# Optimization experiments

Hardware: AMD Instinct MI355X
Metric: run time of the kernel (lower is better)

Reference implementation:

```python
import jax, jax.numpy as jnp
import numpy as np

B, L, D = 32768, 256, 16  # batch, chain length, bond dim; physical dim d=2


def setup_inputs() -> dict:
    key = jax.random.key(0)
    k_phi, k_first, k_mid, k_last = jax.random.split(key, 4)
    scale = 1.0 / np.sqrt(2.0 * D)  # variance-preserving chain
    phi_batch = jax.random.normal(k_phi, (B, L, 2), dtype=jnp.float32)
    core_first = jax.random.normal(k_first, (2, D), dtype=jnp.float32) * scale
    cores_mid = jax.random.normal(k_mid, (L - 2, D, 2, D), dtype=jnp.float32) * scale
    core_last = jax.random.normal(k_last, (D, 2), dtype=jnp.float32) * scale
    out_bias = jnp.zeros((), dtype=jnp.float32)
    return {
        "phi_batch": phi_batch,
        "core_first": core_first,
        "cores_mid": cores_mid,
        "core_last": core_last,
        "out_bias": out_bias,
    }


def reference(phi_batch, core_first, cores_mid, core_last, out_bias):
    # MPS / tensor-train contraction, batched over samples.
    # Each sample contracts feature vectors phi[i] (len-2) into the physical
    # index of core i, then chains the resulting D x D matrices via a
    # left-to-right bond-space matvec (what cotengra would find per-sample).
    # v0: [B, D] = phi[:,0] contracted with first core [2, D]
    v0 = jnp.einsum("bp,pd->bd", phi_batch[:, 0], core_first)

    # middle features, scan-major layout: [L-2, B, 2]
    phis_mid = jnp.swapaxes(phi_batch[:, 1:-1], 0, 1)

    def step(v, xs):
        phi_t, core = xs  # phi_t: [B, 2], core: [D, 2, D]
        # contract bond then physical index; never materialize [B, D, D]
        u = jnp.einsum("bq,qpr->bpr", v, core)   # [B, 2, D]
        v_new = jnp.einsum("bp,bpr->br", phi_t, u)  # [B, D]
        return v_new, None

    v, _ = jax.lax.scan(step, v0, (phis_mid, cores_mid))

    # close the chain with last core [D, 2] and last feature [B, 2]
    out = jnp.einsum("bq,qp,bp->b", v, core_last, phi_batch[:, -1])
    return out + out_bias
```

## Files before the change

### kernel.cpp

```cpp
#include <hip/hip_runtime.h>
#include <stdint.h>


typedef short  bf16x8 __attribute__((ext_vector_type(8)));
typedef float  f32x4  __attribute__((ext_vector_type(4)));
typedef int    i32x4  __attribute__((ext_vector_type(4)));
typedef unsigned int u32;

#define NPF 64
#define NPB 63
#define BWD_OFF (NPF*4*64)

#define PACK_HI(hi, lo) ((int)__builtin_amdgcn_perm((u32)(hi), (u32)(lo), 0x07060302u))

__device__ __forceinline__ u32 rne_bump(u32 u){ return u + 0x7FFFu + ((u >> 16) & 1u); }

__global__ void build_pair_frags(const float* __restrict__ cm, i32x4* __restrict__ ws)
{
  __shared__ float Ca[512], Cb[512];
  const int bid = blockIdx.x;
  const bool fwd = bid < NPF;
  const int j  = fwd ? bid : bid - NPF;
  const int ta = fwd ? 2*j     : 252 - 2*j;
  const int tb = fwd ? 2*j + 1 : 253 - 2*j;
  {
    const float* A = cm + ta*512;
    const float* B = cm + tb*512;
    for (int i = threadIdx.x; i < 512; i += 256){ Ca[i] = A[i]; Cb[i] = B[i]; }
  }
  __syncthreads();
  const int f    = threadIdx.x >> 6;
  const int lane = threadIdx.x & 63;
  const int m    = lane & 15;
  const int g    = lane >> 4;
  const int p    = f >> 1, q = f & 1;
  u32 hi[4], lo[4];
  #pragma unroll
  for (int x = 0; x < 4; ++x){
    const int cq = 4*g + x;
    float acc = 0.f;
    #pragma unroll
    for (int r = 0; r < 16; ++r){
      const float a = fwd ? Ca[cq*32 + p*16 + r] : Ca[m*32 + p*16 + r];
      const float b = fwd ? Cb[r*32 + q*16 + m]  : Cb[r*32 + q*16 + cq];
      acc = fmaf(a, b, acc);
    }
    const u32 u  = __float_as_uint(acc);
    const u32 aa = rne_bump(u);
    const float hf = __uint_as_float(aa & 0xFFFF0000u);
    const u32 bb = rne_bump(__float_as_uint(acc - hf));
    hi[x] = aa >> 16; lo[x] = bb >> 16;
  }
  i32x4 w;
  w[0] = (int)(hi[0] | (hi[1] << 16));
  w[1] = (int)(hi[2] | (hi[3] << 16));
  w[2] = (int)(lo[0] | (lo[1] << 16));
  w[3] = (int)(lo[2] | (lo[3] << 16));
  ws[(fwd ? 0 : BWD_OFF) + (j*4 + f)*64 + lane] = w;
}

__global__ __launch_bounds__(256, 4) void mps_chain(
  const float* __restrict__ phi,
  const float* __restrict__ core_first,
  const float* __restrict__ core_last,
  const float* __restrict__ bias,
  const i32x4* __restrict__ ws,
  float* __restrict__ out)
{
  const int lane = threadIdx.x & 63;
  const int wv   = threadIdx.x >> 6;
  const int b0   = blockIdx.x * 32;
  const int n    = lane & 15;
  const int g    = lane >> 4;
  const int half = wv & 1;
  const int s_in = half*16 + n;
  const bool isFwd = (wv < 2);
  const int dirIdx = isFwd ? 0 : 1;

  __shared__ float red[64*20];

  const float* phiRow = phi + (size_t)(b0 + s_in) * 512;

  const float* phiSrc = phi + (size_t)(b0 + 16*half + (lane & 15)) * 512
                            + (lane >> 4) * 4;

  const i32x4* wsD    = isFwd ? ws : (ws + BWD_OFF);
  const int    maxPr  = isFwd ? NPF - 1 : NPB - 1;
  const i32x4* wsLane = wsD + lane;

  const int qtF  = isFwd ? 0 : 1;
  const int aQ   = ((lane & 15) + 16*qtF) << 2;
  const int adrA0 = isFwd ? aQ       : aQ + 64;
  const int adrB0 = isFwd ? aQ + 64  : aQ + 128;
  const int adrA1 = isFwd ? aQ + 64  : aQ;
  const int adrB1 = isFwd ? aQ + 128 : aQ + 64;

  float v[4];
  i32x4 bfr;

  auto make_bfrag = [&](){
    const u32 u0 = __float_as_uint(v[0]), u1 = __float_as_uint(v[1]);
    const u32 u2 = __float_as_uint(v[2]), u3 = __float_as_uint(v[3]);
    const float l0 = v[0] - __uint_as_float(u0 & 0xFFFF0000u);
    const float l1 = v[1] - __uint_as_float(u1 & 0xFFFF0000u);
    const float l2 = v[2] - __uint_as_float(u2 & 0xFFFF0000u);
    const float l3 = v[3] - __uint_as_float(u3 & 0xFFFF0000u);
    bfr[0] = PACK_HI(u1, u0);
    bfr[1] = PACK_HI(u3, u2);
    bfr[2] = PACK_HI(__float_as_uint(l1), __float_as_uint(l0));
    bfr[3] = PACK_HI(__float_as_uint(l3), __float_as_uint(l2));
  };

  auto pair_step = [&](const i32x4& G0, const i32x4& G1, const i32x4& G2,
                       const i32x4& G3, float2 cA, float2 cB){
    const float c00 = cA.x*cB.x, c01 = cA.x*cB.y;
    const float c10 = cA.y*cB.x, c11 = cA.y*cB.y;
    i32x4 sw; sw[0]=bfr[2]; sw[1]=bfr[3]; sw[2]=bfr[0]; sw[3]=bfr[1];
    const bf16x8 bh = __builtin_bit_cast(bf16x8, bfr);
    const bf16x8 bs = __builtin_bit_cast(bf16x8, sw);
    const f32x4 z = {0.f,0.f,0.f,0.f};
    __builtin_amdgcn_s_setprio(1);
    f32x4 a00 = __builtin_amdgcn_mfma_f32_16x16x32_bf16(__builtin_bit_cast(bf16x8,G0), bh, z, 0,0,0);
    a00 = __builtin_amdgcn_mfma_f32_16x16x32_bf16(__builtin_bit_cast(bf16x8,G0), bs, a00, 0,0,0);
    f32x4 a01 = __builtin_amdgcn_mfma_f32_16x16x32_bf16(__builtin_bit_cast(bf16x8,G1), bh, z, 0,0,0);
    a01 = __builtin_amdgcn_mfma_f32_16x16x32_bf16(__builtin_bit_cast(bf16x8,G1), bs, a01, 0,0,0);
    f32x4 a10 = __builtin_amdgcn_mfma_f32_16x16x32_bf16(__builtin_bit_cast(bf16x8,G2), bh, z, 0,0,0);
    a10 = __builtin_amdgcn_mfma_f32_16x16x32_bf16(__builtin_bit_cast(bf16x8,G2), bs, a10, 0,0,0);
    f32x4 a11 = __builtin_amdgcn_mfma_f32_16x16x32_bf16(__builtin_bit_cast(bf16x8,G3), bh, z, 0,0,0);
    a11 = __builtin_amdgcn_mfma_f32_16x16x32_bf16(__builtin_bit_cast(bf16x8,G3), bs, a11, 0,0,0);
    __builtin_amdgcn_s_setprio(0);
    #pragma unroll
    for (int i2 = 0; i2 < 4; ++i2)
      v[i2] = c00*a00[i2] + c01*a01[i2] + c10*a10[i2] + c11*a11[i2];
    make_bfrag();
  };

  if (isFwd){
    const float2 ph0 = *(const float2*)phiRow;
    #pragma unroll
    for (int reg = 0; reg < 4; ++reg){
      const int r = g*4 + reg;
      v[reg] = ph0.x * core_first[r] + ph0.y * core_first[16 + r];
    }
  } else {
    const float2 phL2 = *(const float2*)(phiRow + 510);
    #pragma unroll
    for (int reg = 0; reg < 4; ++reg){
      const int r = g*4 + reg;
      v[reg] = phL2.x * core_last[2*r] + phL2.y * core_last[2*r + 1];
    }
  }
  make_bfrag();

  i32x4 A0, A1, A2, A3;
  i32x4 B0, B1, B2, B3;
  f32x4 phiC, phiN;

  {
    const i32x4* s = wsLane;
    A0 = s[0]; A1 = s[64]; A2 = s[128]; A3 = s[192];
  }
  {
    const i32x4* s = wsLane + 256;
    B0 = s[0]; B1 = s[64]; B2 = s[128]; B3 = s[192];
  }
  phiC = *(const f32x4*)(phiSrc + (isFwd ? 0 : 496));
  phiN = *(const f32x4*)(phiSrc + (isFwd ? 8 : 488));

  #pragma unroll 1
  for (int c = 0; c < 32; ++c){
    auto S = [&](int e, int adr)->float {
      return __int_as_float(__builtin_amdgcn_ds_bpermute(adr, __float_as_int(phiC[e])));
    };
    const float2 xA0 = make_float2(S(2, adrA0), S(3, adrA0));
    const float2 xB0 = make_float2(S(0, adrB0), S(1, adrB0));
    const float2 xA1 = make_float2(S(2, adrA1), S(3, adrA1));
    const float2 xB1 = make_float2(S(0, adrB1), S(1, adrB1));

    pair_step(A0, A1, A2, A3, xA0, xB0);
    {
      const int j = 2*c + 2;
      const i32x4* s = wsLane + (j > maxPr ? maxPr : j) * 256;
      A0 = s[0]; A1 = s[64]; A2 = s[128]; A3 = s[192];
    }

    if (isFwd || (2*c + 1) < NPB)
      pair_step(B0, B1, B2, B3, xA1, xB1);
    {
      const int j = 2*c + 3;
      const i32x4* s = wsLane + (j > maxPr ? maxPr : j) * 256;
      B0 = s[0]; B1 = s[64]; B2 = s[128]; B3 = s[192];
    }

    phiC = phiN;
    {
      const int cc = (c + 2 > 31) ? 31 : (c + 2);
      phiN = *(const f32x4*)(phiSrc + (isFwd ? 8*cc : 496 - 8*cc));
    }
  }

  *(float4*)&red[(dirIdx*32 + s_in)*20 + 4*g] =
      make_float4(v[0], v[1], v[2], v[3]);
  __syncthreads();
  if (threadIdx.x < 32){
    const int s = threadIdx.x;
    float acc = bias[0];
    #pragma unroll
    for (int qq = 0; qq < 16; ++qq)
      acc += red[s*20 + qq] * red[(32 + s)*20 + qq];
    out[b0 + s] = acc;
  }
}

extern "C" void kernel_launch(void* const* d_in, const int* in_sizes, int n_in,
                              void* d_out, int out_size, void* d_ws, size_t ws_size,
                              hipStream_t stream)
{
  const float* phi  = (const float*)d_in[0];
  const float* cf   = (const float*)d_in[1];
  const float* cm   = (const float*)d_in[2];
  const float* cl   = (const float*)d_in[3];
  const float* bias = (const float*)d_in[4];
  i32x4* ws = (i32x4*)d_ws;

  build_pair_frags<<<NPF + NPB, 256, 0, stream>>>(cm, ws);
  mps_chain<<<1024, 256, 0, stream>>>(phi, cf, cl, bias, ws, (float*)d_out);
}
```

Baseline: 148.4 us.

## Process four independent sample chains per wave to reuse core fragments and hide MFMA latency

Each wave now carries four 16-sample chains instead of one. The pair-core MFMA fragments loaded from the workspace are reused across all four, and the four independent dependency chains give the scheduler ILP to cover MFMA latency. The grid drops from 1024 to 256 blocks and launch bounds change to 1 block per CU. It also removes setprio, adds sched_barriers, and enlarges the reduction buffer. On 256 CUs this is one block per CU with only 4 waves each, which risks low occupancy and more register pressure.

```diff
diff --git a/kernel.cpp b/kernel.cpp
--- a/kernel.cpp
+++ b/kernel.cpp
@@ -59,7 +59,45 @@
   ws[(fwd ? 0 : BWD_OFF) + (j*4 + f)*64 + lane] = w;
 }
 
-__global__ __launch_bounds__(256, 4) void mps_chain(
+__device__ __forceinline__ void make_bfrag(const float (&v)[4], i32x4 &bfr)
+{
+  const u32 u0 = __float_as_uint(v[0]), u1 = __float_as_uint(v[1]);
+  const u32 u2 = __float_as_uint(v[2]), u3 = __float_as_uint(v[3]);
+  const float l0 = v[0] - __uint_as_float(u0 & 0xFFFF0000u);
+  const float l1 = v[1] - __uint_as_float(u1 & 0xFFFF0000u);
+  const float l2 = v[2] - __uint_as_float(u2 & 0xFFFF0000u);
+  const float l3 = v[3] - __uint_as_float(u3 & 0xFFFF0000u);
+  bfr[0] = PACK_HI(u1, u0);
+  bfr[1] = PACK_HI(u3, u2);
+  bfr[2] = PACK_HI(__float_as_uint(l1), __float_as_uint(l0));
+  bfr[3] = PACK_HI(__float_as_uint(l3), __float_as_uint(l2));
+}
+
+__device__ __forceinline__ void pair_step(
+    const i32x4 &G0, const i32x4 &G1, const i32x4 &G2, const i32x4 &G3,
+    float2 cA, float2 cB, float (&v)[4], i32x4 &bfr)
+{
+  const float c00 = cA.x*cB.x, c01 = cA.x*cB.y;
+  const float c10 = cA.y*cB.x, c11 = cA.y*cB.y;
+  i32x4 sw; sw[0]=bfr[2]; sw[1]=bfr[3]; sw[2]=bfr[0]; sw[3]=bfr[1];
+  const bf16x8 bh = __builtin_bit_cast(bf16x8, bfr);
+  const bf16x8 bs = __builtin_bit_cast(bf16x8, sw);
+  const f32x4 z = {0.f,0.f,0.f,0.f};
+  f32x4 a00 = __builtin_amdgcn_mfma_f32_16x16x32_bf16(__builtin_bit_cast(bf16x8,G0), bh, z, 0,0,0);
+  a00 = __builtin_amdgcn_mfma_f32_16x16x32_bf16(__builtin_bit_cast(bf16x8,G0), bs, a00, 0,0,0);
+  f32x4 a01 = __builtin_amdgcn_mfma_f32_16x16x32_bf16(__builtin_bit_cast(bf16x8,G1), bh, z, 0,0,0);
+  a01 = __builtin_amdgcn_mfma_f32_16x16x32_bf16(__builtin_bit_cast(bf16x8,G1), bs, a01, 0,0,0);
+  f32x4 a10 = __builtin_amdgcn_mfma_f32_16x16x32_bf16(__builtin_bit_cast(bf16x8,G2), bh, z, 0,0,0);
+  a10 = __builtin_amdgcn_mfma_f32_16x16x32_bf16(__builtin_bit_cast(bf16x8,G2), bs, a10, 0,0,0);
+  f32x4 a11 = __builtin_amdgcn_mfma_f32_16x16x32_bf16(__builtin_bit_cast(bf16x8,G3), bh, z, 0,0,0);
+  a11 = __builtin_amdgcn_mfma_f32_16x16x32_bf16(__builtin_bit_cast(bf16x8,G3), bs, a11, 0,0,0);
+  #pragma unroll
+  for (int i2 = 0; i2 < 4; ++i2)
+    v[i2] = c00*a00[i2] + c01*a01[i2] + c10*a10[i2] + c11*a11[i2];
+  make_bfrag(v, bfr);
+}
+
+__global__ __launch_bounds__(256, 1) void mps_chain(
   const float* __restrict__ phi,
   const float* __restrict__ core_first,
   const float* __restrict__ core_last,
@@ -69,24 +107,19 @@
 {
   const int lane = threadIdx.x & 63;
   const int wv   = threadIdx.x >> 6;
-  const int b0   = blockIdx.x * 32;
   const int n    = lane & 15;
   const int g    = lane >> 4;
-  const int half = wv & 1;
-  const int s_in = half*16 + n;
   const bool isFwd = (wv < 2);
   const int dirIdx = isFwd ? 0 : 1;
-
-  __shared__ float red[64*20];
-
-  const float* phiRow = phi + (size_t)(b0 + s_in) * 512;
-
-  const float* phiSrc = phi + (size_t)(b0 + 16*half + (lane & 15)) * 512
-                            + (lane >> 4) * 4;
+  const int sb   = blockIdx.x * 128 + (wv & 1) * 64;
+
+  __shared__ float red[256*20];
 
   const i32x4* wsD    = isFwd ? ws : (ws + BWD_OFF);
   const int    maxPr  = isFwd ? NPF - 1 : NPB - 1;
   const i32x4* wsLane = wsD + lane;
+
+  const float* phiSrc0 = phi + (size_t)(sb + n) * 512 + g * 4;
 
   const int qtF  = isFwd ? 0 : 1;
   const int aQ   = ((lane & 15) + 16*qtF) << 2;
@@ -95,120 +128,97 @@
   const int adrA1 = isFwd ? aQ + 64  : aQ;
   const int adrB1 = isFwd ? aQ + 128 : aQ + 64;
 
-  float v[4];
-  i32x4 bfr;
-
-  auto make_bfrag = [&](){
-    const u32 u0 = __float_as_uint(v[0]), u1 = __float_as_uint(v[1]);
-    const u32 u2 = __float_as_uint(v[2]), u3 = __float_as_uint(v[3]);
-    const float l0 = v[0] - __uint_as_float(u0 & 0xFFFF0000u);
-    const float l1 = v[1] - __uint_as_float(u1 & 0xFFFF0000u);
-    const float l2 = v[2] - __uint_as_float(u2 & 0xFFFF0000u);
-    const float l3 = v[3] - __uint_as_float(u3 & 0xFFFF0000u);
-    bfr[0] = PACK_HI(u1, u0);
-    bfr[1] = PACK_HI(u3, u2);
-    bfr[2] = PACK_HI(__float_as_uint(l1), __float_as_uint(l0));
-    bfr[3] = PACK_HI(__float_as_uint(l3), __float_as_uint(l2));
-  };
-
-  auto pair_step = [&](const i32x4& G0, const i32x4& G1, const i32x4& G2,
-                       const i32x4& G3, float2 cA, float2 cB){
-    const float c00 = cA.x*cB.x, c01 = cA.x*cB.y;
-    const float c10 = cA.y*cB.x, c11 = cA.y*cB.y;
-    i32x4 sw; sw[0]=bfr[2]; sw[1]=bfr[3]; sw[2]=bfr[0]; sw[3]=bfr[1];
-    const bf16x8 bh = __builtin_bit_cast(bf16x8, bfr);
-    const bf16x8 bs = __builtin_bit_cast(bf16x8, sw);
-    const f32x4 z = {0.f,0.f,0.f,0.f};
-    __builtin_amdgcn_s_setprio(1);
-    f32x4 a00 = __builtin_amdgcn_mfma_f32_16x16x32_bf16(__builtin_bit_cast(bf16x8,G0), bh, z, 0,0,0);
-    a00 = __builtin_amdgcn_mfma_f32_16x16x32_bf16(__builtin_bit_cast(bf16x8,G0), bs, a00, 0,0,0);
-    f32x4 a01 = __builtin_amdgcn_mfma_f32_16x16x32_bf16(__builtin_bit_cast(bf16x8,G1), bh, z, 0,0,0);
-    a01 = __builtin_amdgcn_mfma_f32_16x16x32_bf16(__builtin_bit_cast(bf16x8,G1), bs, a01, 0,0,0);
-    f32x4 a10 = __builtin_amdgcn_mfma_f32_16x16x32_bf16(__builtin_bit_cast(bf16x8,G2), bh, z, 0,0,0);
-    a10 = __builtin_amdgcn_mfma_f32_16x16x32_bf16(__builtin_bit_cast(bf16x8,G2), bs, a10, 0,0,0);
-    f32x4 a11 = __builtin_amdgcn_mfma_f32_16x16x32_bf16(__builtin_bit_cast(bf16x8,G3), bh, z, 0,0,0);
-    a11 = __builtin_amdgcn_mfma_f32_16x16x32_bf16(__builtin_bit_cast(bf16x8,G3), bs, a11, 0,0,0);
-    __builtin_amdgcn_s_setprio(0);
-    #pragma unroll
-    for (int i2 = 0; i2 < 4; ++i2)
-      v[i2] = c00*a00[i2] + c01*a01[i2] + c10*a10[i2] + c11*a11[i2];
-    make_bfrag();
-  };
-
-  if (isFwd){
-    const float2 ph0 = *(const float2*)phiRow;
-    #pragma unroll
-    for (int reg = 0; reg < 4; ++reg){
-      const int r = g*4 + reg;
-      v[reg] = ph0.x * core_first[r] + ph0.y * core_first[16 + r];
-    }
-  } else {
-    const float2 phL2 = *(const float2*)(phiRow + 510);
-    #pragma unroll
-    for (int reg = 0; reg < 4; ++reg){
-      const int r = g*4 + reg;
-      v[reg] = phL2.x * core_last[2*r] + phL2.y * core_last[2*r + 1];
-    }
-  }
-  make_bfrag();
-
-  i32x4 A0, A1, A2, A3;
-  i32x4 B0, B1, B2, B3;
-  f32x4 phiC, phiN;
-
-  {
-    const i32x4* s = wsLane;
-    A0 = s[0]; A1 = s[64]; A2 = s[128]; A3 = s[192];
-  }
-  {
-    const i32x4* s = wsLane + 256;
-    B0 = s[0]; B1 = s[64]; B2 = s[128]; B3 = s[192];
-  }
-  phiC = *(const f32x4*)(phiSrc + (isFwd ? 0 : 496));
-  phiN = *(const f32x4*)(phiSrc + (isFwd ? 8 : 488));
+  float vch[4][4];
+  i32x4 bfr[4];
+
+  #pragma unroll
+  for (int k = 0; k < 4; ++k){
+    const float* pr = phi + (size_t)(sb + 16*k + n) * 512;
+    if (isFwd){
+      const float2 p0 = *(const float2*)pr;
+      #pragma unroll
+      for (int reg = 0; reg < 4; ++reg){
+        const int r = g*4 + reg;
+        vch[k][reg] = p0.x * core_first[r] + p0.y * core_first[16 + r];
+      }
+    } else {
+      const float2 pL = *(const float2*)(pr + 510);
+      #pragma unroll
+      for (int reg = 0; reg < 4; ++reg){
+        const int r = g*4 + reg;
+        vch[k][reg] = pL.x * core_last[2*r] + pL.y * core_last[2*r + 1];
+      }
+    }
+    make_bfrag(vch[k], bfr[k]);
+  }
+
+  i32x4 GA0, GA1, GA2, GA3;
+  i32x4 GB0, GB1, GB2, GB3;
+  f32x4 phiC[4], phiN[4];
+
+  { const i32x4* s = wsLane;        GA0=s[0]; GA1=s[64]; GA2=s[128]; GA3=s[192]; }
+  { const i32x4* s = wsLane + 256;  GB0=s[0]; GB1=s[64]; GB2=s[128]; GB3=s[192]; }
+  #pragma unroll
+  for (int k = 0; k < 4; ++k){
+    const float* ps = phiSrc0 + (size_t)k * 16 * 512;
+    phiC[k] = *(const f32x4*)(ps + (isFwd ? 0 : 496));
+    phiN[k] = *(const f32x4*)(ps + (isFwd ? 8 : 488));
+  }
+  __builtin_amdgcn_sched_barrier(0);
 
   #pragma unroll 1
   for (int c = 0; c < 32; ++c){
-    auto S = [&](int e, int adr)->float {
-      return __int_as_float(__builtin_amdgcn_ds_bpermute(adr, __float_as_int(phiC[e])));
-    };
-    const float2 xA0 = make_float2(S(2, adrA0), S(3, adrA0));
-    const float2 xB0 = make_float2(S(0, adrB0), S(1, adrB0));
-    const float2 xA1 = make_float2(S(2, adrA1), S(3, adrA1));
-    const float2 xB1 = make_float2(S(0, adrB1), S(1, adrB1));
-
-    pair_step(A0, A1, A2, A3, xA0, xB0);
-    {
-      const int j = 2*c + 2;
+    float2 cA0[4], cB0[4], cA1[4], cB1[4];
+    #pragma unroll
+    for (int k = 0; k < 4; ++k){
+      #define SPULL(e, adr) __int_as_float(__builtin_amdgcn_ds_bpermute((adr), __float_as_int(phiC[k][e])))
+      cA0[k] = make_float2(SPULL(2, adrA0), SPULL(3, adrA0));
+      cB0[k] = make_float2(SPULL(0, adrB0), SPULL(1, adrB0));
+      cA1[k] = make_float2(SPULL(2, adrA1), SPULL(3, adrA1));
+      cB1[k] = make_float2(SPULL(0, adrB1), SPULL(1, adrB1));
+      #undef SPULL
+    }
+
+    #pragma unroll
+    for (int k = 0; k < 4; ++k)
+      pair_step(GA0, GA1, GA2, GA3, cA0[k], cB0[k], vch[k], bfr[k]);
+    { const int j = 2*c + 2;
       const i32x4* s = wsLane + (j > maxPr ? maxPr : j) * 256;
-      A0 = s[0]; A1 = s[64]; A2 = s[128]; A3 = s[192];
-    }
-
-    if (isFwd || (2*c + 1) < NPB)
-      pair_step(B0, B1, B2, B3, xA1, xB1);
-    {
-      const int j = 2*c + 3;
+      GA0=s[0]; GA1=s[64]; GA2=s[128]; GA3=s[192]; }
+    __builtin_amdgcn_sched_barrier(0);
+
+    if (isFwd || (2*c + 1) < NPB){
+      #pragma unroll
+      for (int k = 0; k < 4; ++k)
+        pair_step(GB0, GB1, GB2, GB3, cA1[k], cB1[k], vch[k], bfr[k]);
+    }
+    { const int j = 2*c + 3;
       const i32x4* s = wsLane + (j > maxPr ? maxPr : j) * 256;
-      B0 = s[0]; B1 = s[64]; B2 = s[128]; B3 = s[192];
-    }
-
-    phiC = phiN;
-    {
-      const int cc = (c + 2 > 31) ? 31 : (c + 2);
-      phiN = *(const f32x4*)(phiSrc + (isFwd ? 8*cc : 496 - 8*cc));
-    }
-  }
-
-  *(float4*)&red[(dirIdx*32 + s_in)*20 + 4*g] =
-      make_float4(v[0], v[1], v[2], v[3]);
+      GB0=s[0]; GB1=s[64]; GB2=s[128]; GB3=s[192]; }
+
+    #pragma unroll
+    for (int k = 0; k < 4; ++k) phiC[k] = phiN[k];
+    { const int cc = (c + 2 > 31) ? 31 : (c + 2);
+      #pragma unroll
+      for (int k = 0; k < 4; ++k){
+        const float* ps = phiSrc0 + (size_t)k * 16 * 512;
+        phiN[k] = *(const f32x4*)(ps + (isFwd ? 8*cc : 496 - 8*cc));
+      } }
+    __builtin_amdgcn_sched_barrier(0);
+  }
+
+  #pragma unroll
+  for (int k = 0; k < 4; ++k)
+    *(float4*)&red[(dirIdx*128 + (wv & 1)*64 + 16*k + n)*20 + 4*g] =
+        make_float4(vch[k][0], vch[k][1], vch[k][2], vch[k][3]);
   __syncthreads();
-  if (threadIdx.x < 32){
+  if (threadIdx.x < 128){
     const int s = threadIdx.x;
     float acc = bias[0];
     #pragma unroll
     for (int qq = 0; qq < 16; ++qq)
-      acc += red[s*20 + qq] * red[(32 + s)*20 + qq];
-    out[b0 + s] = acc;
+      acc += red[s*20 + qq] * red[(128 + s)*20 + qq];
+    out[blockIdx.x*128 + s] = acc;
   }
 }
 
@@ -224,5 +234,5 @@
   i32x4* ws = (i32x4*)d_ws;
 
   build_pair_frags<<<NPF + NPB, 256, 0, stream>>>(cm, ws);
-  mps_chain<<<1024, 256, 0, stream>>>(phi, cf, cl, bias, ws, (float*)d_out);
-}
+  mps_chain<<<256, 256, 0, stream>>>(phi, cf, cl, bias, ws, (float*)d_out);
+}
```

Result: no change. 145.5 us (-2.0%).

## Deepen fragment prefetch to three stages with explicit vmcnt waits

Applied to the files above, without the earlier changes.

Restructures the chain loop so it handles four pair-steps per iteration, rotating four fragment register sets and two phi buffers. Loads are issued about three steps ahead, with s_waitcnt vmcnt(9) and sched_barrier pinning the order. The aim is to hide global/L2 latency of the per-step core fragments, which sat on the serial dependency chain with only one step of lookahead. In exchange it uses more VGPRs, which may hurt occupancy under launch_bounds(256,4), and relies on hand-counted waitcnts being correct.

```diff
diff --git a/kernel.cpp b/kernel.cpp
--- a/kernel.cpp
+++ b/kernel.cpp
@@ -59,6 +59,50 @@
   ws[(fwd ? 0 : BWD_OFF) + (j*4 + f)*64 + lane] = w;
 }
 
+__device__ __forceinline__ void make_bfrag(const float (&v)[4], i32x4 &bfr)
+{
+  const u32 u0 = __float_as_uint(v[0]), u1 = __float_as_uint(v[1]);
+  const u32 u2 = __float_as_uint(v[2]), u3 = __float_as_uint(v[3]);
+  const float l0 = v[0] - __uint_as_float(u0 & 0xFFFF0000u);
+  const float l1 = v[1] - __uint_as_float(u1 & 0xFFFF0000u);
+  const float l2 = v[2] - __uint_as_float(u2 & 0xFFFF0000u);
+  const float l3 = v[3] - __uint_as_float(u3 & 0xFFFF0000u);
+  bfr[0] = PACK_HI(u1, u0);
+  bfr[1] = PACK_HI(u3, u2);
+  bfr[2] = PACK_HI(__float_as_uint(l1), __float_as_uint(l0));
+  bfr[3] = PACK_HI(__float_as_uint(l3), __float_as_uint(l2));
+}
+
+__device__ __forceinline__ void pair_step(
+    const i32x4 &G0, const i32x4 &G1, const i32x4 &G2, const i32x4 &G3,
+    float2 cA, float2 cB, float (&v)[4], i32x4 &bfr)
+{
+  const float c00 = cA.x*cB.x, c01 = cA.x*cB.y;
+  const float c10 = cA.y*cB.x, c11 = cA.y*cB.y;
+  i32x4 sw; sw[0]=bfr[2]; sw[1]=bfr[3]; sw[2]=bfr[0]; sw[3]=bfr[1];
+  const bf16x8 bh = __builtin_bit_cast(bf16x8, bfr);
+  const bf16x8 bs = __builtin_bit_cast(bf16x8, sw);
+  const f32x4 z = {0.f,0.f,0.f,0.f};
+  __builtin_amdgcn_s_setprio(1);
+  f32x4 a00 = __builtin_amdgcn_mfma_f32_16x16x32_bf16(__builtin_bit_cast(bf16x8,G0), bh, z, 0,0,0);
+  a00 = __builtin_amdgcn_mfma_f32_16x16x32_bf16(__builtin_bit_cast(bf16x8,G0), bs, a00, 0,0,0);
+  f32x4 a01 = __builtin_amdgcn_mfma_f32_16x16x32_bf16(__builtin_bit_cast(bf16x8,G1), bh, z, 0,0,0);
+  a01 = __builtin_amdgcn_mfma_f32_16x16x32_bf16(__builtin_bit_cast(bf16x8,G1), bs, a01, 0,0,0);
+  f32x4 a10 = __builtin_amdgcn_mfma_f32_16x16x32_bf16(__builtin_bit_cast(bf16x8,G2), bh, z, 0,0,0);
+  a10 = __builtin_amdgcn_mfma_f32_16x16x32_bf16(__builtin_bit_cast(bf16x8,G2), bs, a10, 0,0,0);
+  f32x4 a11 = __builtin_amdgcn_mfma_f32_16x16x32_bf16(__builtin_bit_cast(bf16x8,G3), bh, z, 0,0,0);
+  a11 = __builtin_amdgcn_mfma_f32_16x16x32_bf16(__builtin_bit_cast(bf16x8,G3), bs, a11, 0,0,0);
+  __builtin_amdgcn_s_setprio(0);
+  #pragma unroll
+  for (int i2 = 0; i2 < 4; ++i2)
+    v[i2] = c00*a00[i2] + c01*a01[i2] + c10*a10[i2] + c11*a11[i2];
+  make_bfrag(v, bfr);
+}
+
+#define WAIT9 do { asm volatile("s_waitcnt vmcnt(9)" ::: "memory"); \
+                   __builtin_amdgcn_sched_barrier(0); } while(0)
+#define SB    __builtin_amdgcn_sched_barrier(0)
+
 __global__ __launch_bounds__(256, 4) void mps_chain(
   const float* __restrict__ phi,
   const float* __restrict__ core_first,
@@ -80,7 +124,6 @@
   __shared__ float red[64*20];
 
   const float* phiRow = phi + (size_t)(b0 + s_in) * 512;
-
   const float* phiSrc = phi + (size_t)(b0 + 16*half + (lane & 15)) * 512
                             + (lane >> 4) * 4;
 
@@ -98,43 +141,6 @@
   float v[4];
   i32x4 bfr;
 
-  auto make_bfrag = [&](){
-    const u32 u0 = __float_as_uint(v[0]), u1 = __float_as_uint(v[1]);
-    const u32 u2 = __float_as_uint(v[2]), u3 = __float_as_uint(v[3]);
-    const float l0 = v[0] - __uint_as_float(u0 & 0xFFFF0000u);
-    const float l1 = v[1] - __uint_as_float(u1 & 0xFFFF0000u);
-    const float l2 = v[2] - __uint_as_float(u2 & 0xFFFF0000u);
-    const float l3 = v[3] - __uint_as_float(u3 & 0xFFFF0000u);
-    bfr[0] = PACK_HI(u1, u0);
-    bfr[1] = PACK_HI(u3, u2);
-    bfr[2] = PACK_HI(__float_as_uint(l1), __float_as_uint(l0));
-    bfr[3] = PACK_HI(__float_as_uint(l3), __float_as_uint(l2));
-  };
-
-  auto pair_step = [&](const i32x4& G0, const i32x4& G1, const i32x4& G2,
-                       const i32x4& G3, float2 cA, float2 cB){
-    const float c00 = cA.x*cB.x, c01 = cA.x*cB.y;
-    const float c10 = cA.y*cB.x, c11 = cA.y*cB.y;
-    i32x4 sw; sw[0]=bfr[2]; sw[1]=bfr[3]; sw[2]=bfr[0]; sw[3]=bfr[1];
-    const bf16x8 bh = __builtin_bit_cast(bf16x8, bfr);
-    const bf16x8 bs = __builtin_bit_cast(bf16x8, sw);
-    const f32x4 z = {0.f,0.f,0.f,0.f};
-    __builtin_amdgcn_s_setprio(1);
-    f32x4 a00 = __builtin_amdgcn_mfma_f32_16x16x32_bf16(__builtin_bit_cast(bf16x8,G0), bh, z, 0,0,0);
-    a00 = __builtin_amdgcn_mfma_f32_16x16x32_bf16(__builtin_bit_cast(bf16x8,G0), bs, a00, 0,0,0);
-    f32x4 a01 = __builtin_amdgcn_mfma_f32_16x16x32_bf16(__builtin_bit_cast(bf16x8,G1), bh, z, 0,0,0);
-    a01 = __builtin_amdgcn_mfma_f32_16x16x32_bf16(__builtin_bit_cast(bf16x8,G1), bs, a01, 0,0,0);
-    f32x4 a10 = __builtin_amdgcn_mfma_f32_16x16x32_bf16(__builtin_bit_cast(bf16x8,G2), bh, z, 0,0,0);
-    a10 = __builtin_amdgcn_mfma_f32_16x16x32_bf16(__builtin_bit_cast(bf16x8,G2), bs, a10, 0,0,0);
-    f32x4 a11 = __builtin_amdgcn_mfma_f32_16x16x32_bf16(__builtin_bit_cast(bf16x8,G3), bh, z, 0,0,0);
-    a11 = __builtin_amdgcn_mfma_f32_16x16x32_bf16(__builtin_bit_cast(bf16x8,G3), bs, a11, 0,0,0);
-    __builtin_amdgcn_s_setprio(0);
-    #pragma unroll
-    for (int i2 = 0; i2 < 4; ++i2)
-      v[i2] = c00*a00[i2] + c01*a01[i2] + c10*a10[i2] + c11*a11[i2];
-    make_bfrag();
-  };
-
   if (isFwd){
     const float2 ph0 = *(const float2*)phiRow;
     #pragma unroll
@@ -150,54 +156,57 @@
       v[reg] = phL2.x * core_last[2*r] + phL2.y * core_last[2*r + 1];
     }
   }
-  make_bfrag();
-
-  i32x4 A0, A1, A2, A3;
-  i32x4 B0, B1, B2, B3;
-  f32x4 phiC, phiN;
-
-  {
-    const i32x4* s = wsLane;
-    A0 = s[0]; A1 = s[64]; A2 = s[128]; A3 = s[192];
-  }
-  {
-    const i32x4* s = wsLane + 256;
-    B0 = s[0]; B1 = s[64]; B2 = s[128]; B3 = s[192];
-  }
-  phiC = *(const f32x4*)(phiSrc + (isFwd ? 0 : 496));
-  phiN = *(const f32x4*)(phiSrc + (isFwd ? 8 : 488));
+  make_bfrag(v, bfr);
+
+  i32x4 S0g0,S0g1,S0g2,S0g3, S1g0,S1g1,S1g2,S1g3;
+  i32x4 S2g0,S2g1,S2g2,S2g3, S3g0,S3g1,S3g2,S3g3;
+  f32x4 P0, P1;
+
+  #define FRAG_LOAD(S, j) do { \
+    const i32x4* s_ = wsLane + ((j) > maxPr ? maxPr : (j)) * 256; \
+    S##g0 = s_[0]; S##g1 = s_[64]; S##g2 = s_[128]; S##g3 = s_[192]; } while(0)
+
+  #define PHI_LOAD(P, cn) do { \
+    const int cc_ = (cn) > 31 ? 31 : (cn); \
+    P = *(const f32x4*)(phiSrc + (isFwd ? 8*cc_ : 496 - 8*cc_)); } while(0)
+
+  #define SPULL(P, e, adr) __int_as_float(__builtin_amdgcn_ds_bpermute((adr), __float_as_int(P[e])))
+  #define COEFFS(P, xA0_, xB0_, xA1_, xB1_) do { \
+    xA0_ = make_float2(SPULL(P,2,adrA0), SPULL(P,3,adrA0)); \
+    xB0_ = make_float2(SPULL(P,0,adrB0), SPULL(P,1,adrB0)); \
+    xA1_ = make_float2(SPULL(P,2,adrA1), SPULL(P,3,adrA1)); \
+    xB1_ = make_float2(SPULL(P,0,adrB1), SPULL(P,1,adrB1)); } while(0)
+
+  PHI_LOAD(P0, 0);
+  FRAG_LOAD(S0, 0);
+  FRAG_LOAD(S1, 1);
+  PHI_LOAD(P1, 1);
+  FRAG_LOAD(S2, 2);
+  SB;
 
   #pragma unroll 1
-  for (int c = 0; c < 32; ++c){
-    auto S = [&](int e, int adr)->float {
-      return __int_as_float(__builtin_amdgcn_ds_bpermute(adr, __float_as_int(phiC[e])));
-    };
-    const float2 xA0 = make_float2(S(2, adrA0), S(3, adrA0));
-    const float2 xB0 = make_float2(S(0, adrB0), S(1, adrB0));
-    const float2 xA1 = make_float2(S(2, adrA1), S(3, adrA1));
-    const float2 xB1 = make_float2(S(0, adrB1), S(1, adrB1));
-
-    pair_step(A0, A1, A2, A3, xA0, xB0);
-    {
-      const int j = 2*c + 2;
-      const i32x4* s = wsLane + (j > maxPr ? maxPr : j) * 256;
-      A0 = s[0]; A1 = s[64]; A2 = s[128]; A3 = s[192];
-    }
-
-    if (isFwd || (2*c + 1) < NPB)
-      pair_step(B0, B1, B2, B3, xA1, xB1);
-    {
-      const int j = 2*c + 3;
-      const i32x4* s = wsLane + (j > maxPr ? maxPr : j) * 256;
-      B0 = s[0]; B1 = s[64]; B2 = s[128]; B3 = s[192];
-    }
-
-    phiC = phiN;
-    {
-      const int cc = (c + 2 > 31) ? 31 : (c + 2);
-      phiN = *(const f32x4*)(phiSrc + (isFwd ? 8*cc : 496 - 8*cc));
-    }
-  }
+  for (int t = 0; t < 16; ++t){
+    float2 c0A, c0B, c1A, c1B, d0A, d0B, d1A, d1B;
+
+    WAIT9;
+    COEFFS(P0, c0A, c0B, c1A, c1B);
+    pair_step(S0g0,S0g1,S0g2,S0g3, c0A, c0B, v, bfr);
+    FRAG_LOAD(S3, 4*t + 3); SB;
+    WAIT9;
+    pair_step(S1g0,S1g1,S1g2,S1g3, c1A, c1B, v, bfr);
+    PHI_LOAD(P0, 2*t + 2); FRAG_LOAD(S0, 4*t + 4); SB;
+    WAIT9;
+    COEFFS(P1, d0A, d0B, d1A, d1B);
+    pair_step(S2g0,S2g1,S2g2,S2g3, d0A, d0B, v, bfr);
+    FRAG_LOAD(S1, 4*t + 5); SB;
+    WAIT9;
+    if (isFwd || (4*t + 3) < NPB)
+      pair_step(S3g0,S3g1,S3g2,S3g3, d1A, d1B, v, bfr);
+    PHI_LOAD(P1, 2*t + 3); FRAG_LOAD(S2, 4*t + 6); SB;
+  }
+
+  asm volatile("s_waitcnt vmcnt(0)" ::: "memory");
+  __builtin_amdgcn_sched_barrier(0);
 
   *(float4*)&red[(dirIdx*32 + s_in)*20 + 4*g] =
       make_float4(v[0], v[1], v[2], v[3]);
@@ -210,6 +219,11 @@
       acc += red[s*20 + qq] * red[(32 + s)*20 + qq];
     out[b0 + s] = acc;
   }
+
+  #undef FRAG_LOAD
+  #undef PHI_LOAD
+  #undef SPULL
+  #undef COEFFS
 }
 
 extern "C" void kernel_launch(void* const* d_in, const int* in_sizes, int n_in,
```

Measured after the change: 150.0 us. Within noise of the previous version (+1.1%).
